# Kernel tuning notes

Measured on AMD Instinct MI355X. Metric: run time of the kernel, lower is better.

## Reference

```python
import jax, jax.numpy as jnp
import numpy as np

N_NODES = 50000


def _gcn_layer(x, src, dst, deg_inv_sqrt, W, b):
    # GCNConv (PyG defaults): h = x @ W; out = D^-1/2 (A+I) D^-1/2 h + b
    h = x @ W
    norm = deg_inv_sqrt[src] * deg_inv_sqrt[dst]          # [E]
    msg = h[src] * norm[:, None]                           # [E, d_out]
    agg = jax.ops.segment_sum(msg, dst, num_segments=N_NODES)
    agg = agg + h * (deg_inv_sqrt * deg_inv_sqrt)[:, None]  # self-loop term
    return agg + b


def _stack(x, src, dst, dis, W1, b1, W2, b2, W3, b3):
    h = jax.nn.relu(_gcn_layer(x, src, dst, dis, W1, b1))
    h = jax.nn.relu(_gcn_layer(h, src, dst, dis, W2, b2))
    return jax.nn.relu(_gcn_layer(h, src, dst, dis, W3, b3))


def setup_inputs() -> dict:
    key = jax.random.key(0)
    ks = jax.random.split(key, 16)
    din, lat, E = 128, 64, 800000
    x = jax.random.normal(ks[0], (N_NODES, din), dtype=jnp.float32)
    edge_index = jax.random.randint(ks[1], (2, E), 0, N_NODES, dtype=jnp.int64)

    def lin(k, fan_in, fan_out):
        s = 1.0 / np.sqrt(fan_in)
        kw, kb = jax.random.split(k)
        W = jax.random.uniform(kw, (fan_in, fan_out), minval=-s, maxval=s, dtype=jnp.float32)
        b = jax.random.uniform(kb, (fan_out,), minval=-s, maxval=s, dtype=jnp.float32)
        return W, b

    Wm1, bm1 = lin(ks[2], din, 64)
    Wm2, bm2 = lin(ks[3], 64, 128)
    Wm3, bm3 = lin(ks[4], 128, lat)
    Wl1, bl1 = lin(ks[5], din, 64)
    Wl2, bl2 = lin(ks[6], 64, 128)
    Wl3, bl3 = lin(ks[7], 128, lat)
    return {"x": x, "edge_index": edge_index,
            "Wm1": Wm1, "bm1": bm1, "Wm2": Wm2, "bm2": bm2, "Wm3": Wm3, "bm3": bm3,
            "Wl1": Wl1, "bl1": bl1, "Wl2": Wl2, "bl2": bl2, "Wl3": Wl3, "bl3": bl3}


def reference(x, edge_index, Wm1, bm1, Wm2, bm2, Wm3, bm3, Wl1, bl1, Wl2, bl2, Wl3, bl3):
    src, dst = edge_index[0], edge_index[1]
    # degree with self-loops (PyG: deg over dst of A+I)
    deg = jax.ops.segment_sum(jnp.ones_like(dst, dtype=x.dtype), dst, num_segments=N_NODES) + 1.0
    dis = jax.lax.rsqrt(deg)
    mu = _stack(x, src, dst, dis, Wm1, bm1, Wm2, bm2, Wm3, bm3)
    log = _stack(x, src, dst, dis, Wl1, bl1, Wl2, bl2, Wl3, bl3)
    return (mu, log)
```

## Files before the change

kernel.cpp:

```cpp
#include <hip/hip_runtime.h>

#define N_NODES_C 50000

__global__ void detect_kernel(const int* __restrict__ w, int ncheck, int* __restrict__ flag) {
    int tid = blockIdx.x * blockDim.x + threadIdx.x;
    if (tid < ncheck) {
        if (w[2 * tid + 1] != 0) *flag = 0;
    }
}

__global__ void count_kernel(const int* __restrict__ ei, int E, const int* __restrict__ flag,
                             int* __restrict__ counts) {
    int e = blockIdx.x * blockDim.x + threadIdx.x;
    if (e >= E) return;
    int shift = (*flag != 0) ? 1 : 0;
    int d = ei[(unsigned)(E + e) << shift];
    atomicAdd(&counts[d], 1);
}

__global__ void dis_kernel(const int* __restrict__ counts, float* __restrict__ dis, int n) {
    int i = blockIdx.x * blockDim.x + threadIdx.x;
    if (i < n) dis[i] = rsqrtf((float)counts[i] + 1.0f);
}

__global__ void scan_kernel(const int* __restrict__ counts, int* __restrict__ row_start,
                            int* __restrict__ cursor, int n) {
    __shared__ int wsum[16];
    __shared__ int carry;
    __shared__ int chunk_total;
    int tid = threadIdx.x;
    int lane = tid & 63;
    int wid = tid >> 6;
    if (tid == 0) carry = 0;
    __syncthreads();
    for (int base = 0; base < n; base += 1024) {
        int i = base + tid;
        int v = (i < n) ? counts[i] : 0;
        int x = v;
        #pragma unroll
        for (int off = 1; off < 64; off <<= 1) {
            int y = __shfl_up(x, off);
            if (lane >= off) x += y;
        }
        if (lane == 63) wsum[wid] = x;
        __syncthreads();
        if (tid == 0) {
            int run = 0;
            #pragma unroll
            for (int q = 0; q < 16; q++) { int t = wsum[q]; wsum[q] = run; run += t; }
            chunk_total = run;
        }
        __syncthreads();
        int excl = x - v + wsum[wid] + carry;
        if (i < n) { row_start[i] = excl; cursor[i] = excl; }
        __syncthreads();
        if (tid == 0) carry += chunk_total;
        __syncthreads();
    }
    if (tid == 0) row_start[n] = carry;
}

__global__ void fill_kernel(const int* __restrict__ ei, int E, const int* __restrict__ flag,
                            const float* __restrict__ dis, int* __restrict__ cursor,
                            int* __restrict__ csr_src, float* __restrict__ csr_w) {
    int e = blockIdx.x * blockDim.x + threadIdx.x;
    if (e >= E) return;
    int shift = (*flag != 0) ? 1 : 0;
    int s = ei[(unsigned)e << shift];
    int d = ei[(unsigned)(E + e) << shift];
    int pos = atomicAdd(&cursor[d], 1);
    csr_src[pos] = s;
    csr_w[pos] = dis[s] * dis[d];
}

template <bool FINAL>
__global__ __launch_bounds__(256) void agg128_kernel(const float* __restrict__ h,
                                                     const int* __restrict__ row_start,
                                                     const int* __restrict__ csr_src,
                                                     const float* __restrict__ csr_w,
                                                     const float* __restrict__ dis,
                                                     const float* __restrict__ bmu,
                                                     const float* __restrict__ blog,
                                                     float* __restrict__ out,
                                                     float* __restrict__ outlog, int M) {
    int wid = threadIdx.x >> 6;
    int lane = threadIdx.x & 63;
    int node = blockIdx.x * 4 + wid;
    if (node >= M) return;
    int half = lane >> 5;
    int c0 = (lane & 31) * 4;

    int s = row_start[node];
    int e = row_start[node + 1];

    float a0 = 0.f, a1 = 0.f, a2 = 0.f, a3 = 0.f;
    int i = s + half;
    for (; i + 2 < e; i += 4) {
        int s0 = csr_src[i];
        int s1 = csr_src[i + 2];
        float w0 = csr_w[i];
        float w1 = csr_w[i + 2];
        float4 v0 = *(const float4*)&h[(size_t)s0 * 128 + c0];
        float4 v1 = *(const float4*)&h[(size_t)s1 * 128 + c0];
        a0 = fmaf(w0, v0.x, a0); a1 = fmaf(w0, v0.y, a1);
        a2 = fmaf(w0, v0.z, a2); a3 = fmaf(w0, v0.w, a3);
        a0 = fmaf(w1, v1.x, a0); a1 = fmaf(w1, v1.y, a1);
        a2 = fmaf(w1, v1.z, a2); a3 = fmaf(w1, v1.w, a3);
    }
    if (i < e) {
        int s0 = csr_src[i];
        float w0 = csr_w[i];
        float4 v0 = *(const float4*)&h[(size_t)s0 * 128 + c0];
        a0 = fmaf(w0, v0.x, a0); a1 = fmaf(w0, v0.y, a1);
        a2 = fmaf(w0, v0.z, a2); a3 = fmaf(w0, v0.w, a3);
    }
    a0 += __shfl_xor(a0, 32);
    a1 += __shfl_xor(a1, 32);
    a2 += __shfl_xor(a2, 32);
    a3 += __shfl_xor(a3, 32);

    float dn = dis[node];
    float sw = dn * dn;
    float4 sv = *(const float4*)&h[(size_t)node * 128 + c0];
    a0 = fmaf(sw, sv.x, a0); a1 = fmaf(sw, sv.y, a1);
    a2 = fmaf(sw, sv.z, a2); a3 = fmaf(sw, sv.w, a3);

    if (half == 0) {
        if constexpr (FINAL) {
            float b0, b1, b2, b3;
            float* yp;
            if (c0 < 64) {
                b0 = bmu[c0]; b1 = bmu[c0 + 1]; b2 = bmu[c0 + 2]; b3 = bmu[c0 + 3];
                yp = out + (size_t)node * 64 + c0;
            } else {
                int c = c0 - 64;
                b0 = blog[c]; b1 = blog[c + 1]; b2 = blog[c + 2]; b3 = blog[c + 3];
                yp = outlog + (size_t)node * 64 + c;
            }
            float4 o;
            o.x = fmaxf(a0 + b0, 0.f);
            o.y = fmaxf(a1 + b1, 0.f);
            o.z = fmaxf(a2 + b2, 0.f);
            o.w = fmaxf(a3 + b3, 0.f);
            *(float4*)yp = o;
        } else {
            *(float4*)&out[(size_t)node * 128 + c0] = make_float4(a0, a1, a2, a3);
        }
    }
}

template <int K, int N, bool CAT, bool RELU, bool BIAS>
__global__ __launch_bounds__(256) void gemm_kernel(const float* __restrict__ X, int ldx,
                                                   const float* __restrict__ Wa,
                                                   const float* __restrict__ Wb,
                                                   const float* __restrict__ ba,
                                                   const float* __restrict__ bb,
                                                   float* __restrict__ Y, int ldy, int M) {
    constexpr int BM = 32;
    constexpr int KCH = (K > 64) ? 64 : K;
    constexpr int XLD = K + 4;
    constexpr int NTX = N / 4;
    constexpr int NTY = 256 / NTX;
    constexpr int RPT = BM / NTY;
    __shared__ alignas(16) float xs[BM * XLD];
    __shared__ alignas(16) float ws[KCH * N];

    int t = threadIdx.x;
    int row0 = blockIdx.x * BM;

    constexpr int KQ = K / 4;
    for (int i = t; i < BM * KQ; i += 256) {
        int r = i / KQ, kq = i % KQ;
        float4 v = make_float4(0.f, 0.f, 0.f, 0.f);
        if (row0 + r < M) v = *(const float4*)&X[(size_t)(row0 + r) * ldx + 4 * kq];
        *(float4*)&xs[r * XLD + 4 * kq] = v;
    }

    int tx = t % NTX;
    int ty = t / NTX;
    float acc[RPT][4];
    #pragma unroll
    for (int rr = 0; rr < RPT; rr++)
        #pragma unroll
        for (int j = 0; j < 4; j++) acc[rr][j] = 0.f;

    for (int kc = 0; kc < K; kc += KCH) {
        __syncthreads();
        constexpr int NQ = N / 4;
        if constexpr (CAT) {
            constexpr int HQ = (N / 2) / 4;
            for (int i = t; i < KCH * NQ; i += 256) {
                int kk = i / NQ, cq = i % NQ;
                float4 v;
                if (cq < HQ) v = *(const float4*)&Wa[(size_t)(kc + kk) * (N / 2) + 4 * cq];
                else         v = *(const float4*)&Wb[(size_t)(kc + kk) * (N / 2) + 4 * (cq - HQ)];
                *(float4*)&ws[kk * N + 4 * cq] = v;
            }
        } else {
            for (int i = t; i < KCH * NQ; i += 256) {
                int kk = i / NQ, cq = i % NQ;
                *(float4*)&ws[kk * N + 4 * cq] =
                    *(const float4*)&Wa[(size_t)(kc + kk) * N + 4 * cq];
            }
        }
        __syncthreads();

        #pragma unroll 4
        for (int kk = 0; kk < KCH; ++kk) {
            int k = kc + kk;
            float4 wv = *(const float4*)&ws[kk * N + tx * 4];
            float xv[RPT];
            #pragma unroll
            for (int rr = 0; rr < RPT; rr++) xv[rr] = xs[(ty * RPT + rr) * XLD + k];
            #pragma unroll
            for (int rr = 0; rr < RPT; rr++) {
                acc[rr][0] = fmaf(xv[rr], wv.x, acc[rr][0]);
                acc[rr][1] = fmaf(xv[rr], wv.y, acc[rr][1]);
                acc[rr][2] = fmaf(xv[rr], wv.z, acc[rr][2]);
                acc[rr][3] = fmaf(xv[rr], wv.w, acc[rr][3]);
            }
        }
    }

    int c0 = tx * 4;
    float b0 = 0.f, b1 = 0.f, b2 = 0.f, b3 = 0.f;
    if constexpr (BIAS) {
        if constexpr (CAT) {
            if (c0 < N / 2) { b0 = ba[c0]; b1 = ba[c0 + 1]; b2 = ba[c0 + 2]; b3 = ba[c0 + 3]; }
            else {
                int c = c0 - N / 2;
                b0 = bb[c]; b1 = bb[c + 1]; b2 = bb[c + 2]; b3 = bb[c + 3];
            }
        } else {
            b0 = ba[c0]; b1 = ba[c0 + 1]; b2 = ba[c0 + 2]; b3 = ba[c0 + 3];
        }
    }
    #pragma unroll
    for (int rr = 0; rr < RPT; rr++) {
        int row = row0 + ty * RPT + rr;
        if (row < M) {
            float4 o;
            o.x = acc[rr][0] + b0;
            o.y = acc[rr][1] + b1;
            o.z = acc[rr][2] + b2;
            o.w = acc[rr][3] + b3;
            if constexpr (RELU) {
                o.x = fmaxf(o.x, 0.f); o.y = fmaxf(o.y, 0.f);
                o.z = fmaxf(o.z, 0.f); o.w = fmaxf(o.w, 0.f);
            }
            *(float4*)&Y[(size_t)row * ldy + c0] = o;
        }
    }
}

extern "C" void kernel_launch(void* const* d_in, const int* in_sizes, int n_in,
                              void* d_out, int out_size, void* d_ws, size_t ws_size,
                              hipStream_t stream) {
    const float* x   = (const float*)d_in[0];
    const int*   ei  = (const int*)d_in[1];
    const float* Wm1 = (const float*)d_in[2];  const float* bm1 = (const float*)d_in[3];
    const float* Wm2 = (const float*)d_in[4];  const float* bm2 = (const float*)d_in[5];
    const float* Wm3 = (const float*)d_in[6];  const float* bm3 = (const float*)d_in[7];
    const float* Wl1 = (const float*)d_in[8];  const float* bl1 = (const float*)d_in[9];
    const float* Wl2 = (const float*)d_in[10]; const float* bl2 = (const float*)d_in[11];
    const float* Wl3 = (const float*)d_in[12]; const float* bl3 = (const float*)d_in[13];
    float* out = (float*)d_out;

    const int M = N_NODES_C;
    const int E = in_sizes[1] / 2;

    char* ws = (char*)d_ws;
    size_t off = 0;
    auto alloc = [&](size_t bytes) {
        size_t o = off;
        off += (bytes + 255) & ~(size_t)255;
        return o;
    };
    int*   flag      = (int*)(ws + alloc(4));
    int*   counts    = (int*)(ws + alloc((size_t)M * 4));
    int*   row_start = (int*)(ws + alloc((size_t)(M + 1) * 4));
    int*   cursor    = (int*)(ws + alloc((size_t)M * 4));
    float* dis       = (float*)(ws + alloc((size_t)M * 4));
    int*   csr_src   = (int*)(ws + alloc((size_t)E * 4));
    float* csr_w     = (float*)(ws + alloc((size_t)E * 4));
    float* bufA      = (float*)(ws + alloc((size_t)M * 256 * 4));
    float* bufB      = (float*)(ws + alloc((size_t)M * 256 * 4));

    hipMemsetAsync(flag, 1, 4, stream);
    hipMemsetAsync(counts, 0, (size_t)M * 4, stream);

    int ncheck = (E < 2048) ? E : 2048;
    detect_kernel<<<(ncheck + 255) / 256, 256, 0, stream>>>(ei, ncheck, flag);
    count_kernel<<<(E + 255) / 256, 256, 0, stream>>>(ei, E, flag, counts);
    dis_kernel<<<(M + 255) / 256, 256, 0, stream>>>(counts, dis, M);
    scan_kernel<<<1, 1024, 0, stream>>>(counts, row_start, cursor, M);
    fill_kernel<<<(E + 255) / 256, 256, 0, stream>>>(ei, E, flag, dis, cursor, csr_src, csr_w);

    int gblocks = (M + 31) / 32;
    int ablocks = (M + 3) / 4;

    agg128_kernel<false><<<ablocks, 256, 0, stream>>>(x, row_start, csr_src, csr_w, dis,
                                                      nullptr, nullptr, bufA, nullptr, M);
    gemm_kernel<128, 128, true, true, true><<<gblocks, 256, 0, stream>>>(
        bufA, 128, Wm1, Wl1, bm1, bl1, bufB, 128, M);

    agg128_kernel<false><<<ablocks, 256, 0, stream>>>(bufB, row_start, csr_src, csr_w, dis,
                                                      nullptr, nullptr, bufA, nullptr, M);
    gemm_kernel<64, 128, false, true, true><<<gblocks, 256, 0, stream>>>(
        bufA, 128, Wm2, nullptr, bm2, nullptr, bufB, 256, M);
    gemm_kernel<64, 128, false, true, true><<<gblocks, 256, 0, stream>>>(
        bufA + 64, 128, Wl2, nullptr, bl2, nullptr, bufB + 128, 256, M);

    gemm_kernel<128, 64, false, false, false><<<gblocks, 256, 0, stream>>>(
        bufB, 256, Wm3, nullptr, nullptr, nullptr, bufA, 128, M);
    gemm_kernel<128, 64, false, false, false><<<gblocks, 256, 0, stream>>>(
        bufB + 128, 256, Wl3, nullptr, nullptr, nullptr, bufA + 64, 128, M);

    agg128_kernel<true><<<ablocks, 256, 0, stream>>>(bufA, row_start, csr_src, csr_w, dis,
                                                     bm3, bl3, out, out + (size_t)M * 64, M);
}
```

Before: 520.6 us.

## Fuse mu/log branch GEMMs into single dual-weight kernels with 8-wide register tiles

Replaces the generic GEMM with a dual-branch kernel that computes both the mu and log branch outputs in one launch. Each thread now produces 4 columns from each half, reading the input row once when both halves share it, or at two offsets otherwise. The layer-2 and layer-3 GEMM pairs become one launch each, and layer 1 moves to 64-row tiles with 32-wide K chunks. This cuts launches and makes better use of each staged input tile, at the cost of higher register pressure. It also adds a zeroed bias buffer so layer 3 can reuse the bias path.

```diff
diff --git a/kernel.cpp b/kernel.cpp
--- a/kernel.cpp
+++ b/kernel.cpp
@@ -149,106 +149,97 @@
     }
 }
 
-template <int K, int N, bool CAT, bool RELU, bool BIAS>
-__global__ __launch_bounds__(256) void gemm_kernel(const float* __restrict__ X, int ldx,
-                                                   const float* __restrict__ Wa,
-                                                   const float* __restrict__ Wb,
-                                                   const float* __restrict__ ba,
-                                                   const float* __restrict__ bb,
-                                                   float* __restrict__ Y, int ldy, int M) {
-    constexpr int BM = 32;
-    constexpr int KCH = (K > 64) ? 64 : K;
-    constexpr int XLD = K + 4;
-    constexpr int NTX = N / 4;
+template <int K, int N, int LDXS, int XA, int XB, int BM, int KCH, bool RELU>
+__global__ __launch_bounds__(256) void gemm2_kernel(const float* __restrict__ X,
+                                                    const float* __restrict__ Wa,
+                                                    const float* __restrict__ Wb,
+                                                    const float* __restrict__ ba,
+                                                    const float* __restrict__ bb,
+                                                    float* __restrict__ Y, int ldy, int M) {
+    constexpr int NTX = N / 8;
     constexpr int NTY = 256 / NTX;
     constexpr int RPT = BM / NTY;
+    constexpr int XLD = LDXS + 4;
+    constexpr int NH = N / 2;
     __shared__ alignas(16) float xs[BM * XLD];
     __shared__ alignas(16) float ws[KCH * N];
 
     int t = threadIdx.x;
     int row0 = blockIdx.x * BM;
 
-    constexpr int KQ = K / 4;
+    constexpr int KQ = LDXS / 4;
     for (int i = t; i < BM * KQ; i += 256) {
         int r = i / KQ, kq = i % KQ;
         float4 v = make_float4(0.f, 0.f, 0.f, 0.f);
-        if (row0 + r < M) v = *(const float4*)&X[(size_t)(row0 + r) * ldx + 4 * kq];
+        if (row0 + r < M) v = *(const float4*)&X[(size_t)(row0 + r) * LDXS + 4 * kq];
         *(float4*)&xs[r * XLD + 4 * kq] = v;
     }
 
     int tx = t % NTX;
     int ty = t / NTX;
-    float acc[RPT][4];
+    float acc[RPT][8];
     #pragma unroll
     for (int rr = 0; rr < RPT; rr++)
         #pragma unroll
-        for (int j = 0; j < 4; j++) acc[rr][j] = 0.f;
+        for (int j = 0; j < 8; j++) acc[rr][j] = 0.f;
 
     for (int kc = 0; kc < K; kc += KCH) {
         __syncthreads();
         constexpr int NQ = N / 4;
-        if constexpr (CAT) {
-            constexpr int HQ = (N / 2) / 4;
-            for (int i = t; i < KCH * NQ; i += 256) {
-                int kk = i / NQ, cq = i % NQ;
-                float4 v;
-                if (cq < HQ) v = *(const float4*)&Wa[(size_t)(kc + kk) * (N / 2) + 4 * cq];
-                else         v = *(const float4*)&Wb[(size_t)(kc + kk) * (N / 2) + 4 * (cq - HQ)];
-                *(float4*)&ws[kk * N + 4 * cq] = v;
-            }
-        } else {
-            for (int i = t; i < KCH * NQ; i += 256) {
-                int kk = i / NQ, cq = i % NQ;
-                *(float4*)&ws[kk * N + 4 * cq] =
-                    *(const float4*)&Wa[(size_t)(kc + kk) * N + 4 * cq];
-            }
+        constexpr int HQ = NH / 4;
+        for (int i = t; i < KCH * NQ; i += 256) {
+            int kk = i / NQ, cq = i % NQ;
+            float4 v;
+            if (cq < HQ) v = *(const float4*)&Wa[(size_t)(kc + kk) * NH + 4 * cq];
+            else         v = *(const float4*)&Wb[(size_t)(kc + kk) * NH + 4 * (cq - HQ)];
+            *(float4*)&ws[kk * N + 4 * cq] = v;
         }
         __syncthreads();
 
         #pragma unroll 4
         for (int kk = 0; kk < KCH; ++kk) {
             int k = kc + kk;
-            float4 wv = *(const float4*)&ws[kk * N + tx * 4];
-            float xv[RPT];
-            #pragma unroll
-            for (int rr = 0; rr < RPT; rr++) xv[rr] = xs[(ty * RPT + rr) * XLD + k];
+            float4 wa = *(const float4*)&ws[kk * N + tx * 4];
+            float4 wb = *(const float4*)&ws[kk * N + NH + tx * 4];
             #pragma unroll
             for (int rr = 0; rr < RPT; rr++) {
-                acc[rr][0] = fmaf(xv[rr], wv.x, acc[rr][0]);
-                acc[rr][1] = fmaf(xv[rr], wv.y, acc[rr][1]);
-                acc[rr][2] = fmaf(xv[rr], wv.z, acc[rr][2]);
-                acc[rr][3] = fmaf(xv[rr], wv.w, acc[rr][3]);
+                int rbase = (ty * RPT + rr) * XLD;
+                float xa = xs[rbase + XA + k];
+                acc[rr][0] = fmaf(xa, wa.x, acc[rr][0]);
+                acc[rr][1] = fmaf(xa, wa.y, acc[rr][1]);
+                acc[rr][2] = fmaf(xa, wa.z, acc[rr][2]);
+                acc[rr][3] = fmaf(xa, wa.w, acc[rr][3]);
+                float xb;
+                if constexpr (XA == XB) xb = xa;
+                else xb = xs[rbase + XB + k];
+                acc[rr][4] = fmaf(xb, wb.x, acc[rr][4]);
+                acc[rr][5] = fmaf(xb, wb.y, acc[rr][5]);
+                acc[rr][6] = fmaf(xb, wb.z, acc[rr][6]);
+                acc[rr][7] = fmaf(xb, wb.w, acc[rr][7]);
             }
         }
     }
 
-    int c0 = tx * 4;
-    float b0 = 0.f, b1 = 0.f, b2 = 0.f, b3 = 0.f;
-    if constexpr (BIAS) {
-        if constexpr (CAT) {
-            if (c0 < N / 2) { b0 = ba[c0]; b1 = ba[c0 + 1]; b2 = ba[c0 + 2]; b3 = ba[c0 + 3]; }
-            else {
-                int c = c0 - N / 2;
-                b0 = bb[c]; b1 = bb[c + 1]; b2 = bb[c + 2]; b3 = bb[c + 3];
-            }
-        } else {
-            b0 = ba[c0]; b1 = ba[c0 + 1]; b2 = ba[c0 + 2]; b3 = ba[c0 + 3];
-        }
-    }
+    int ca = tx * 4;
+    float4 bva = *(const float4*)&ba[ca];
+    float4 bvb = *(const float4*)&bb[ca];
     #pragma unroll
     for (int rr = 0; rr < RPT; rr++) {
         int row = row0 + ty * RPT + rr;
         if (row < M) {
-            float4 o;
-            o.x = acc[rr][0] + b0;
-            o.y = acc[rr][1] + b1;
-            o.z = acc[rr][2] + b2;
-            o.w = acc[rr][3] + b3;
+            float4 oa, ob;
+            oa.x = acc[rr][0] + bva.x; oa.y = acc[rr][1] + bva.y;
+            oa.z = acc[rr][2] + bva.z; oa.w = acc[rr][3] + bva.w;
+            ob.x = acc[rr][4] + bvb.x; ob.y = acc[rr][5] + bvb.y;
+            ob.z = acc[rr][6] + bvb.z; ob.w = acc[rr][7] + bvb.w;
             if constexpr (RELU) {
-                o.x = fmaxf(o.x, 0.f); o.y = fmaxf(o.y, 0.f);
-                o.z = fmaxf(o.z, 0.f); o.w = fmaxf(o.w, 0.f);
+                oa.x = fmaxf(oa.x, 0.f); oa.y = fmaxf(oa.y, 0.f);
+                oa.z = fmaxf(oa.z, 0.f); oa.w = fmaxf(oa.w, 0.f);
+                ob.x = fmaxf(ob.x, 0.f); ob.y = fmaxf(ob.y, 0.f);
+                ob.z = fmaxf(ob.z, 0.f); ob.w = fmaxf(ob.w, 0.f);
             }
-            *(float4*)&Y[(size_t)row * ldy + c0] = o;
+            *(float4*)&Y[(size_t)row * ldy + ca] = oa;
+            *(float4*)&Y[(size_t)row * ldy + NH + ca] = ob;
         }
     }
 }
@@ -296,25 +287,24 @@
     scan_kernel<<<1, 1024, 0, stream>>>(counts, row_start, cursor, M);
     fill_kernel<<<(E + 255) / 256, 256, 0, stream>>>(ei, E, flag, dis, cursor, csr_src, csr_w);
 
-    int gblocks = (M + 31) / 32;
     int ablocks = (M + 3) / 4;
 
     agg128_kernel<false><<<ablocks, 256, 0, stream>>>(x, row_start, csr_src, csr_w, dis,
                                                       nullptr, nullptr, bufA, nullptr, M);
-    gemm_kernel<128, 128, true, true, true><<<gblocks, 256, 0, stream>>>(
-        bufA, 128, Wm1, Wl1, bm1, bl1, bufB, 128, M);
+
+    gemm2_kernel<128, 128, 128, 0, 0, 64, 32, true><<<(M + 63) / 64, 256, 0, stream>>>(
+        bufA, Wm1, Wl1, bm1, bl1, bufB, 128, M);
 
     agg128_kernel<false><<<ablocks, 256, 0, stream>>>(bufB, row_start, csr_src, csr_w, dis,
                                                       nullptr, nullptr, bufA, nullptr, M);
-    gemm_kernel<64, 128, false, true, true><<<gblocks, 256, 0, stream>>>(
-        bufA, 128, Wm2, nullptr, bm2, nullptr, bufB, 256, M);
-    gemm_kernel<64, 128, false, true, true><<<gblocks, 256, 0, stream>>>(
-        bufA + 64, 128, Wl2, nullptr, bl2, nullptr, bufB + 128, 256, M);
-
-    gemm_kernel<128, 64, false, false, false><<<gblocks, 256, 0, stream>>>(
-        bufB, 256, Wm3, nullptr, nullptr, nullptr, bufA, 128, M);
-    gemm_kernel<128, 64, false, false, false><<<gblocks, 256, 0, stream>>>(
-        bufB + 128, 256, Wl3, nullptr, nullptr, nullptr, bufA + 64, 128, M);
+
+    gemm2_kernel<64, 256, 128, 0, 64, 32, 32, true><<<(M + 31) / 32, 256, 0, stream>>>(
+        bufA, Wm2, Wl2, bm2, bl2, bufB, 256, M);
+
+    float* zb = (float*)(ws + alloc(64 * 4));
+    hipMemsetAsync(zb, 0, 64 * 4, stream);
+    gemm2_kernel<128, 128, 256, 0, 128, 32, 32, false><<<(M + 31) / 32, 256, 0, stream>>>(
+        bufB, Wm3, Wl3, zb, zb, bufA, 128, M);
 
     agg128_kernel<true><<<ablocks, 256, 0, stream>>>(bufA, row_start, csr_src, csr_w, dis,
                                                      bm3, bl3, out, out + (size_t)M * 64, M);
```

Measured after the change: 520.2 us. Within noise of the previous version (-0.1%).
